# Performance work log

Hardware: AMD Instinct MI355X
Metric: run time of the kernel (lower is better)

## Reference

```python
import jax, jax.numpy as jnp
import numpy as np

N_NODES = 100000
N_EDGES = 1600000
IN_FEATS = 128
H_FEATS = 64
NUM_CLASSES = 16


def setup_inputs() -> dict:
    key = jax.random.key(0)
    ks = jax.random.split(key, 6)
    X = jax.random.normal(ks[0], (N_NODES, IN_FEATS), dtype=jnp.float32)
    edge_weight = jax.random.uniform(ks[1], (N_EDGES,), dtype=jnp.float32)
    W1 = jax.random.normal(ks[2], (IN_FEATS, H_FEATS), dtype=jnp.float32) * (1.0 / np.sqrt(IN_FEATS))
    b1 = jnp.zeros((H_FEATS,), dtype=jnp.float32)
    W2 = jax.random.normal(ks[3], (H_FEATS, NUM_CLASSES), dtype=jnp.float32) * (1.0 / np.sqrt(H_FEATS))
    b2 = jnp.zeros((NUM_CLASSES,), dtype=jnp.float32)
    edge_src = jax.random.randint(ks[4], (N_EDGES,), 0, N_NODES, dtype=jnp.int32)
    edge_dst = jax.random.randint(ks[5], (N_EDGES,), 0, N_NODES, dtype=jnp.int32)
    return {"X": X, "edge_weight": edge_weight, "W1": W1, "b1": b1,
            "W2": W2, "b2": b2, "edge_src": edge_src, "edge_dst": edge_dst}


def _gcn_conv(H, W, b, edge_src, edge_dst, edge_weight, num_nodes):
    # transform-then-aggregate: out = A @ (H @ W) + b, A given as weighted edge list
    H = H @ W                                  # [N, d_out]
    msgs = H[edge_src] * edge_weight[:, None]  # [E, d_out] gather + scale
    agg = jax.ops.segment_sum(msgs, edge_dst, num_segments=num_nodes)  # scatter-add
    return agg + b


def reference(X, edge_weight, W1, b1, W2, b2, edge_src, edge_dst):
    n = X.shape[0]
    h = jax.nn.relu(_gcn_conv(X, W1, b1, edge_src, edge_dst, edge_weight, n))
    return _gcn_conv(h, W2, b2, edge_src, edge_dst, edge_weight, n)
```

## Files before the change

kernel.cpp:

```cpp
#include <hip/hip_runtime.h>

#define N_NODES 100000
#define N_EDGES 1600000
#define IN_F 128
#define H_F 64
#define C_F 16

#define BIN_SH 7
#define BIN_NODES 128
#define NBINS 782
#define BCAP 2816
#define PART_BLOCKS 391
#define GEMM1_BLOCKS 1563
#define RMAX 6

typedef __attribute__((ext_vector_type(8))) short bf16x8;
typedef __attribute__((ext_vector_type(4))) float f32x4;

__device__ inline unsigned short f2bf(float f) {
  unsigned u = __float_as_uint(f);
  unsigned r = (u + 0x7fff + ((u >> 16) & 1)) >> 16;
  return (unsigned short)r;
}

__global__ __launch_bounds__(256) void part_gemm1_kernel(
    const int* __restrict__ src, const int* __restrict__ dst,
    const float* __restrict__ ew, int* __restrict__ binCnt,
    int2* __restrict__ ebin, const float* __restrict__ X,
    const float* __restrict__ W1, unsigned short* __restrict__ H1b) {
  __shared__ char ldsraw[16 * 1024];
  int tid = threadIdx.x;
  if (blockIdx.x < PART_BLOCKS) {
    int* hist = (int*)ldsraw;
    int* base = hist + NBINS;
    for (int i = tid; i < NBINS; i += 256) hist[i] = 0;
    __syncthreads();
    int i0 = blockIdx.x * 1024;
    int iHi = i0 + 1024;
    if (iHi > N_EDGES / 4) iHi = N_EDGES / 4;
    const int4* d4p = (const int4*)dst;
    const int4* s4p = (const int4*)src;
    const float4* w4p = (const float4*)ew;
    unsigned key[16];
    unsigned aux[16];
#pragma unroll
    for (int it = 0; it < 4; ++it) {
      int i = i0 + it * 256 + tid;
      if (i < iHi) {
        int4 d = d4p[i];
        int4 s = s4p[i];
        float4 w = w4p[i];
#pragma unroll
        for (int j = 0; j < 4; ++j) {
          int dd = (&d.x)[j];
          int ss = (&s.x)[j];
          float ww = (&w.x)[j];
          int bb = dd >> BIN_SH;
          unsigned wf = (unsigned)(ww * 32767.0f + 0.5f);
          key[it * 4 + j] =
              (unsigned)ss | ((unsigned)(dd & (BIN_NODES - 1)) << 17);
          aux[it * 4 + j] = wf | ((unsigned)bb << 15);
          atomicAdd(&hist[bb], 1);
        }
      }
    }
    __syncthreads();
    for (int i = tid; i < NBINS; i += 256)
      base[i] = hist[i] ? atomicAdd(&binCnt[i], hist[i]) : 0;
    __syncthreads();
#pragma unroll
    for (int it = 0; it < 4; ++it) {
      int i = i0 + it * 256 + tid;
      if (i < iHi) {
#pragma unroll
        for (int j = 0; j < 4; ++j) {
          unsigned a = aux[it * 4 + j];
          int bb = (int)(a >> 15);
          int pos = atomicAdd(&base[bb], 1);
          ebin[(size_t)bb * BCAP + pos] =
              make_int2((int)key[it * 4 + j], (int)(a & 0x7FFF));
        }
      }
    }
  } else {
    short* ldsB = (short*)ldsraw;
    for (int idx = tid; idx < 16 * 512; idx += 256) {
      int frag = idx >> 9;
      int entry = idx & 511;
      int lane = entry >> 3, j = entry & 7;
      int c = frag >> 2, s = frag & 3;
      int k = s * 32 + (lane >> 4) * 8 + j;
      int n = c * 16 + (lane & 15);
      ldsB[idx] = (short)f2bf(W1[k * H_F + n]);
    }
    __syncthreads();
    int wave = tid >> 6;
    int lane = tid & 63;
    int rt = (blockIdx.x - PART_BLOCKS) * 4 + wave;
    if (rt >= N_NODES / 16) return;
    int node0 = rt * 16;
    int l = lane & 15, q = lane >> 4;
    const float* xp = X + (size_t)(node0 + l) * IN_F + q * 8;
    f32x4 acc[4] = {f32x4{0.f, 0.f, 0.f, 0.f}, f32x4{0.f, 0.f, 0.f, 0.f},
                    f32x4{0.f, 0.f, 0.f, 0.f}, f32x4{0.f, 0.f, 0.f, 0.f}};
#pragma unroll
    for (int s = 0; s < 4; ++s) {
      float4 x0 = *(const float4*)(xp + s * 32);
      float4 x1 = *(const float4*)(xp + s * 32 + 4);
      bf16x8 a;
      a[0] = f2bf(x0.x); a[1] = f2bf(x0.y); a[2] = f2bf(x0.z); a[3] = f2bf(x0.w);
      a[4] = f2bf(x1.x); a[5] = f2bf(x1.y); a[6] = f2bf(x1.z); a[7] = f2bf(x1.w);
#pragma unroll
      for (int c = 0; c < 4; ++c) {
        bf16x8 b = *(const bf16x8*)&ldsB[(c * 4 + s) * 512 + lane * 8];
        acc[c] = __builtin_amdgcn_mfma_f32_16x16x32_bf16(a, b, acc[c], 0, 0, 0);
      }
    }
#pragma unroll
    for (int c = 0; c < 4; ++c)
#pragma unroll
      for (int r = 0; r < 4; ++r)
        H1b[(size_t)(node0 + q * 4 + r) * H_F + c * 16 + l] = f2bf(acc[c][r]);
  }
}

__global__ __launch_bounds__(512) void gather1s_kernel(
    const uint2* __restrict__ H1q, const int* __restrict__ binCnt,
    const int2* __restrict__ ebin, const float* __restrict__ b1,
    float* __restrict__ agg) {
  __shared__ int h[BIN_NODES], sc[BIN_NODES], cur[BIN_NODES];
  __shared__ unsigned srt[BCAP];
  int b = blockIdx.x, tid = threadIdx.x;
  int lo = b * BCAP;
  int cnt = binCnt[b];
  if (tid < BIN_NODES) h[tid] = 0;
  __syncthreads();
  unsigned rk[RMAX];
  int rd[RMAX];
  int rn = 0;
#pragma unroll
  for (int j = 0; j < RMAX; ++j) {
    int e = j * 512 + tid;
    if (e < cnt) {
      int2 r = ebin[lo + e];
      int dl = (((unsigned)r.x) >> 17) & (BIN_NODES - 1);
      rk[j] = ((unsigned)r.x & 0x1FFFF) | ((unsigned)r.y << 17);
      rd[j] = dl;
      atomicAdd(&h[dl], 1);
      rn = j + 1;
    }
  }
  __syncthreads();
  if (tid < BIN_NODES) sc[tid] = h[tid];
  __syncthreads();
#pragma unroll
  for (int d = 1; d < BIN_NODES; d <<= 1) {
    int t = 0;
    if (tid < BIN_NODES && tid >= d) t = sc[tid - d];
    __syncthreads();
    if (tid < BIN_NODES) sc[tid] += t;
    __syncthreads();
  }
  if (tid < BIN_NODES) cur[tid] = sc[tid] - h[tid];
  __syncthreads();
#pragma unroll
  for (int j = 0; j < RMAX; ++j)
    if (j < rn) {
      int pos = atomicAdd(&cur[rd[j]], 1);
      srt[pos] = rk[j];
    }
  __syncthreads();
  int wv = tid >> 6, lane = tid & 63, g = lane >> 4, li = lane & 15;
  const float wsc = 1.0f / 32767.0f;
  float bb0 = b1[li * 4], bb1 = b1[li * 4 + 1];
  float bb2 = b1[li * 4 + 2], bb3 = b1[li * 4 + 3];
  for (int k = 0; k < 16; ++k) {
    int nl = wv * 16 + k;
    int n = (b << BIN_SH) + nl;
    if (n >= N_NODES) break;
    int e1 = sc[nl], e0 = e1 - h[nl];
    f32x4 a0 = {0.f, 0.f, 0.f, 0.f}, a1 = {0.f, 0.f, 0.f, 0.f};
    f32x4 a2 = {0.f, 0.f, 0.f, 0.f}, a3 = {0.f, 0.f, 0.f, 0.f};
    int i = e0;
    for (; i + 15 < e1; i += 16) {
      unsigned r0 = srt[i + g];
      unsigned r1 = srt[i + 4 + g];
      unsigned r2 = srt[i + 8 + g];
      unsigned r3 = srt[i + 12 + g];
      uint2 v0 = H1q[(r0 & 0x1FFFF) * (H_F / 4) + li];
      uint2 v1 = H1q[(r1 & 0x1FFFF) * (H_F / 4) + li];
      uint2 v2 = H1q[(r2 & 0x1FFFF) * (H_F / 4) + li];
      uint2 v3 = H1q[(r3 & 0x1FFFF) * (H_F / 4) + li];
      float w0 = (float)(r0 >> 17) * wsc, w1 = (float)(r1 >> 17) * wsc;
      float w2 = (float)(r2 >> 17) * wsc, w3 = (float)(r3 >> 17) * wsc;
      a0[0] += __uint_as_float(v0.x << 16) * w0;
      a0[1] += __uint_as_float(v0.x & 0xFFFF0000u) * w0;
      a0[2] += __uint_as_float(v0.y << 16) * w0;
      a0[3] += __uint_as_float(v0.y & 0xFFFF0000u) * w0;
      a1[0] += __uint_as_float(v1.x << 16) * w1;
      a1[1] += __uint_as_float(v1.x & 0xFFFF0000u) * w1;
      a1[2] += __uint_as_float(v1.y << 16) * w1;
      a1[3] += __uint_as_float(v1.y & 0xFFFF0000u) * w1;
      a2[0] += __uint_as_float(v2.x << 16) * w2;
      a2[1] += __uint_as_float(v2.x & 0xFFFF0000u) * w2;
      a2[2] += __uint_as_float(v2.y << 16) * w2;
      a2[3] += __uint_as_float(v2.y & 0xFFFF0000u) * w2;
      a3[0] += __uint_as_float(v3.x << 16) * w3;
      a3[1] += __uint_as_float(v3.x & 0xFFFF0000u) * w3;
      a3[2] += __uint_as_float(v3.y << 16) * w3;
      a3[3] += __uint_as_float(v3.y & 0xFFFF0000u) * w3;
    }
    for (; i + 3 < e1; i += 4) {
      unsigned r0 = srt[i + g];
      uint2 v0 = H1q[(r0 & 0x1FFFF) * (H_F / 4) + li];
      float w0 = (float)(r0 >> 17) * wsc;
      a0[0] += __uint_as_float(v0.x << 16) * w0;
      a0[1] += __uint_as_float(v0.x & 0xFFFF0000u) * w0;
      a0[2] += __uint_as_float(v0.y << 16) * w0;
      a0[3] += __uint_as_float(v0.y & 0xFFFF0000u) * w0;
    }
    if (i + g < e1) {
      unsigned r0 = srt[i + g];
      uint2 v0 = H1q[(r0 & 0x1FFFF) * (H_F / 4) + li];
      float w0 = (float)(r0 >> 17) * wsc;
      a1[0] += __uint_as_float(v0.x << 16) * w0;
      a1[1] += __uint_as_float(v0.x & 0xFFFF0000u) * w0;
      a1[2] += __uint_as_float(v0.y << 16) * w0;
      a1[3] += __uint_as_float(v0.y & 0xFFFF0000u) * w0;
    }
    f32x4 a = (a0 + a1) + (a2 + a3);
#pragma unroll
    for (int c = 0; c < 4; ++c) {
      a[c] += __shfl_xor(a[c], 16, 64);
      a[c] += __shfl_xor(a[c], 32, 64);
    }
    if (g == 0) {
      float4 o;
      o.x = a[0] + bb0;
      o.y = a[1] + bb1;
      o.z = a[2] + bb2;
      o.w = a[3] + bb3;
      *(float4*)&agg[(size_t)n * H_F + li * 4] = o;
    }
  }
}

__global__ __launch_bounds__(256) void gemm2_mfma_kernel(
    const float* __restrict__ agg, const float* __restrict__ W2,
    unsigned short* __restrict__ H2b) {
  __shared__ short ldsB[2 * 512];
  for (int idx = threadIdx.x; idx < 1024; idx += 256) {
    int sfrag = idx >> 9;
    int entry = idx & 511;
    int lane = entry >> 3, j = entry & 7;
    int k = sfrag * 32 + (lane >> 4) * 8 + j;
    int c = lane & 15;
    ldsB[idx] = (short)f2bf(W2[k * C_F + c]);
  }
  __syncthreads();
  int wave = threadIdx.x >> 6;
  int lane = threadIdx.x & 63;
  int rt = blockIdx.x * 4 + wave;
  if (rt >= N_NODES / 16) return;
  int node0 = rt * 16;
  int l = lane & 15, q = lane >> 4;
  const float* ap = agg + (size_t)(node0 + l) * H_F + q * 8;
  f32x4 acc = {0.f, 0.f, 0.f, 0.f};
#pragma unroll
  for (int s = 0; s < 2; ++s) {
    float4 x0 = *(const float4*)(ap + s * 32);
    float4 x1 = *(const float4*)(ap + s * 32 + 4);
    bf16x8 a;
    a[0] = f2bf(fmaxf(x0.x, 0.f)); a[1] = f2bf(fmaxf(x0.y, 0.f));
    a[2] = f2bf(fmaxf(x0.z, 0.f)); a[3] = f2bf(fmaxf(x0.w, 0.f));
    a[4] = f2bf(fmaxf(x1.x, 0.f)); a[5] = f2bf(fmaxf(x1.y, 0.f));
    a[6] = f2bf(fmaxf(x1.z, 0.f)); a[7] = f2bf(fmaxf(x1.w, 0.f));
    bf16x8 bfr = *(const bf16x8*)&ldsB[s * 512 + lane * 8];
    acc = __builtin_amdgcn_mfma_f32_16x16x32_bf16(a, bfr, acc, 0, 0, 0);
  }
#pragma unroll
  for (int r = 0; r < 4; ++r)
    H2b[(size_t)(node0 + q * 4 + r) * C_F + l] = f2bf(acc[r]);
}

__global__ __launch_bounds__(512) void gather2s_kernel(
    const uint2* __restrict__ H2q, const int* __restrict__ binCnt,
    const int2* __restrict__ ebin, const float* __restrict__ b2,
    float* __restrict__ out) {
  __shared__ int h[BIN_NODES], sc[BIN_NODES], cur[BIN_NODES];
  __shared__ unsigned srt[BCAP];
  int b = blockIdx.x, tid = threadIdx.x;
  int lo = b * BCAP;
  int cnt = binCnt[b];
  if (tid < BIN_NODES) h[tid] = 0;
  __syncthreads();
  unsigned rk[RMAX];
  int rd[RMAX];
  int rn = 0;
#pragma unroll
  for (int j = 0; j < RMAX; ++j) {
    int e = j * 512 + tid;
    if (e < cnt) {
      int2 r = ebin[lo + e];
      int dl = (((unsigned)r.x) >> 17) & (BIN_NODES - 1);
      rk[j] = ((unsigned)r.x & 0x1FFFF) | ((unsigned)r.y << 17);
      rd[j] = dl;
      atomicAdd(&h[dl], 1);
      rn = j + 1;
    }
  }
  __syncthreads();
  if (tid < BIN_NODES) sc[tid] = h[tid];
  __syncthreads();
#pragma unroll
  for (int d = 1; d < BIN_NODES; d <<= 1) {
    int t = 0;
    if (tid < BIN_NODES && tid >= d) t = sc[tid - d];
    __syncthreads();
    if (tid < BIN_NODES) sc[tid] += t;
    __syncthreads();
  }
  if (tid < BIN_NODES) cur[tid] = sc[tid] - h[tid];
  __syncthreads();
#pragma unroll
  for (int j = 0; j < RMAX; ++j)
    if (j < rn) {
      int pos = atomicAdd(&cur[rd[j]], 1);
      srt[pos] = rk[j];
    }
  __syncthreads();
  int wv = tid >> 6, lane = tid & 63, g = lane >> 2, li = lane & 3;
  const float wsc = 1.0f / 32767.0f;
  float bb0 = b2[li * 4], bb1 = b2[li * 4 + 1];
  float bb2 = b2[li * 4 + 2], bb3 = b2[li * 4 + 3];
  for (int k = 0; k < 16; ++k) {
    int nl = wv * 16 + k;
    int n = (b << BIN_SH) + nl;
    if (n >= N_NODES) break;
    int e1 = sc[nl], e0 = e1 - h[nl];
    f32x4 a0 = {0.f, 0.f, 0.f, 0.f};
    int i = e0;
    for (; i + 15 < e1; i += 16) {
      unsigned r0 = srt[i + g];
      uint2 v0 = H2q[(r0 & 0x1FFFF) * (C_F / 4) + li];
      float w0 = (float)(r0 >> 17) * wsc;
      a0[0] += __uint_as_float(v0.x << 16) * w0;
      a0[1] += __uint_as_float(v0.x & 0xFFFF0000u) * w0;
      a0[2] += __uint_as_float(v0.y << 16) * w0;
      a0[3] += __uint_as_float(v0.y & 0xFFFF0000u) * w0;
    }
    if (i + g < e1) {
      unsigned r0 = srt[i + g];
      uint2 v0 = H2q[(r0 & 0x1FFFF) * (C_F / 4) + li];
      float w0 = (float)(r0 >> 17) * wsc;
      a0[0] += __uint_as_float(v0.x << 16) * w0;
      a0[1] += __uint_as_float(v0.x & 0xFFFF0000u) * w0;
      a0[2] += __uint_as_float(v0.y << 16) * w0;
      a0[3] += __uint_as_float(v0.y & 0xFFFF0000u) * w0;
    }
#pragma unroll
    for (int c = 0; c < 4; ++c) {
      a0[c] += __shfl_xor(a0[c], 4, 64);
      a0[c] += __shfl_xor(a0[c], 8, 64);
      a0[c] += __shfl_xor(a0[c], 16, 64);
      a0[c] += __shfl_xor(a0[c], 32, 64);
    }
    if (g == 0) {
      float4 o;
      o.x = a0[0] + bb0;
      o.y = a0[1] + bb1;
      o.z = a0[2] + bb2;
      o.w = a0[3] + bb3;
      *(float4*)&out[(size_t)n * C_F + li * 4] = o;
    }
  }
}

extern "C" void kernel_launch(void* const* d_in, const int* in_sizes, int n_in,
                              void* d_out, int out_size, void* d_ws,
                              size_t ws_size, hipStream_t stream) {
  const float* X  = (const float*)d_in[0];
  const float* ew = (const float*)d_in[1];
  const float* W1 = (const float*)d_in[2];
  const float* b1 = (const float*)d_in[3];
  const float* W2 = (const float*)d_in[4];
  const float* b2 = (const float*)d_in[5];
  const int* src  = (const int*)d_in[6];
  const int* dst  = (const int*)d_in[7];
  float* out = (float*)d_out;

  unsigned short* H1b = (unsigned short*)d_ws;
  float* agg  = (float*)((char*)d_ws + (size_t)N_NODES * H_F * 2);
  int2* ebin  = (int2*)((char*)agg + (size_t)N_NODES * H_F * 4);
  int* binCnt = (int*)(ebin + (size_t)NBINS * BCAP);
  unsigned short* H2b = H1b;

  hipMemsetAsync(binCnt, 0, NBINS * sizeof(int), stream);
  part_gemm1_kernel<<<PART_BLOCKS + GEMM1_BLOCKS, 256, 0, stream>>>(
      src, dst, ew, binCnt, ebin, X, W1, H1b);
  gather1s_kernel<<<NBINS, 512, 0, stream>>>((const uint2*)H1b, binCnt, ebin,
                                             b1, agg);
  gemm2_mfma_kernel<<<(N_NODES / 16 + 3) / 4, 256, 0, stream>>>(agg, W2, H2b);
  gather2s_kernel<<<NBINS, 512, 0, stream>>>((const uint2*)H2b, binCnt, ebin,
                                             b2, out);
}
```

Measured before the change: 218.4 us.

## Fuse layer-2 GEMM into layer-1 gather kernel via LDS staging

The layer-1 aggregation kernel now keeps each bin's 128 aggregated node rows in LDS as bias-added, ReLU'd bf16 values. It then runs the 64x16 W2 MFMA directly on them and writes H2 in bf16. This drops the separate gemm2 kernel launch and the round trip of the fp32 agg buffer through global memory (about 25.6 MB written and read). In exchange it adds LDS use (about 18 KB extra per block), which may lower occupancy of the gather kernel, and moves H2b to its own workspace region.

Result: faster. 213.6 us (-2.2%).

```diff
diff --git a/kernel.cpp b/kernel.cpp
--- a/kernel.cpp
+++ b/kernel.cpp
@@ -13,6 +13,7 @@
 #define PART_BLOCKS 391
 #define GEMM1_BLOCKS 1563
 #define RMAX 6
+#define AGG_STRIDE 36
 
 typedef __attribute__((ext_vector_type(8))) short bf16x8;
 typedef __attribute__((ext_vector_type(4))) float f32x4;
@@ -124,13 +125,23 @@
   }
 }
 
-__global__ __launch_bounds__(512) void gather1s_kernel(
+__global__ __launch_bounds__(512) void gather1f_kernel(
     const uint2* __restrict__ H1q, const int* __restrict__ binCnt,
     const int2* __restrict__ ebin, const float* __restrict__ b1,
-    float* __restrict__ agg) {
+    const float* __restrict__ W2, unsigned short* __restrict__ H2b) {
   __shared__ int h[BIN_NODES], sc[BIN_NODES], cur[BIN_NODES];
   __shared__ unsigned srt[BCAP];
+  __shared__ unsigned aggU[BIN_NODES * AGG_STRIDE];
+  __shared__ short ldsW2[2 * 512];
   int b = blockIdx.x, tid = threadIdx.x;
+  for (int idx = tid; idx < 1024; idx += 512) {
+    int sfrag = idx >> 9;
+    int entry = idx & 511;
+    int lane = entry >> 3, j = entry & 7;
+    int k = sfrag * 32 + (lane >> 4) * 8 + j;
+    int c = lane & 15;
+    ldsW2[idx] = (short)f2bf(W2[k * C_F + c]);
+  }
   int lo = b * BCAP;
   int cnt = binCnt[b];
   if (tid < BIN_NODES) h[tid] = 0;
@@ -235,52 +246,31 @@
       a[c] += __shfl_xor(a[c], 32, 64);
     }
     if (g == 0) {
-      float4 o;
-      o.x = a[0] + bb0;
-      o.y = a[1] + bb1;
-      o.z = a[2] + bb2;
-      o.w = a[3] + bb3;
-      *(float4*)&agg[(size_t)n * H_F + li * 4] = o;
-    }
-  }
-}
-
-__global__ __launch_bounds__(256) void gemm2_mfma_kernel(
-    const float* __restrict__ agg, const float* __restrict__ W2,
-    unsigned short* __restrict__ H2b) {
-  __shared__ short ldsB[2 * 512];
-  for (int idx = threadIdx.x; idx < 1024; idx += 256) {
-    int sfrag = idx >> 9;
-    int entry = idx & 511;
-    int lane = entry >> 3, j = entry & 7;
-    int k = sfrag * 32 + (lane >> 4) * 8 + j;
-    int c = lane & 15;
-    ldsB[idx] = (short)f2bf(W2[k * C_F + c]);
-  }
-  __syncthreads();
-  int wave = threadIdx.x >> 6;
-  int lane = threadIdx.x & 63;
-  int rt = blockIdx.x * 4 + wave;
-  if (rt >= N_NODES / 16) return;
-  int node0 = rt * 16;
+      float r0 = fmaxf(a[0] + bb0, 0.f);
+      float r1 = fmaxf(a[1] + bb1, 0.f);
+      float r2 = fmaxf(a[2] + bb2, 0.f);
+      float r3 = fmaxf(a[3] + bb3, 0.f);
+      unsigned p0 = (unsigned)f2bf(r0) | ((unsigned)f2bf(r1) << 16);
+      unsigned p1 = (unsigned)f2bf(r2) | ((unsigned)f2bf(r3) << 16);
+      *(uint2*)&aggU[nl * AGG_STRIDE + li * 2] = make_uint2(p0, p1);
+    }
+  }
+  __syncthreads();
   int l = lane & 15, q = lane >> 4;
-  const float* ap = agg + (size_t)(node0 + l) * H_F + q * 8;
+  int nl0 = wv * 16;
   f32x4 acc = {0.f, 0.f, 0.f, 0.f};
 #pragma unroll
   for (int s = 0; s < 2; ++s) {
-    float4 x0 = *(const float4*)(ap + s * 32);
-    float4 x1 = *(const float4*)(ap + s * 32 + 4);
-    bf16x8 a;
-    a[0] = f2bf(fmaxf(x0.x, 0.f)); a[1] = f2bf(fmaxf(x0.y, 0.f));
-    a[2] = f2bf(fmaxf(x0.z, 0.f)); a[3] = f2bf(fmaxf(x0.w, 0.f));
-    a[4] = f2bf(fmaxf(x1.x, 0.f)); a[5] = f2bf(fmaxf(x1.y, 0.f));
-    a[6] = f2bf(fmaxf(x1.z, 0.f)); a[7] = f2bf(fmaxf(x1.w, 0.f));
-    bf16x8 bfr = *(const bf16x8*)&ldsB[s * 512 + lane * 8];
-    acc = __builtin_amdgcn_mfma_f32_16x16x32_bf16(a, bfr, acc, 0, 0, 0);
-  }
-#pragma unroll
-  for (int r = 0; r < 4; ++r)
-    H2b[(size_t)(node0 + q * 4 + r) * C_F + l] = f2bf(acc[r]);
+    bf16x8 afr = *(const bf16x8*)&aggU[(nl0 + l) * AGG_STRIDE + s * 16 + q * 4];
+    bf16x8 bfr = *(const bf16x8*)&ldsW2[s * 512 + lane * 8];
+    acc = __builtin_amdgcn_mfma_f32_16x16x32_bf16(afr, bfr, acc, 0, 0, 0);
+  }
+  int node0 = (b << BIN_SH) + nl0;
+#pragma unroll
+  for (int r = 0; r < 4; ++r) {
+    int n = node0 + q * 4 + r;
+    if (n < N_NODES) H2b[(size_t)n * C_F + l] = f2bf(acc[r]);
+  }
 }
 
 __global__ __launch_bounds__(512) void gather2s_kernel(
@@ -390,17 +380,15 @@
   float* out = (float*)d_out;
 
   unsigned short* H1b = (unsigned short*)d_ws;
-  float* agg  = (float*)((char*)d_ws + (size_t)N_NODES * H_F * 2);
-  int2* ebin  = (int2*)((char*)agg + (size_t)N_NODES * H_F * 4);
+  unsigned short* H2b = H1b + (size_t)N_NODES * H_F;
+  int2* ebin  = (int2*)(H2b + (size_t)N_NODES * C_F);
   int* binCnt = (int*)(ebin + (size_t)NBINS * BCAP);
-  unsigned short* H2b = H1b;
 
   hipMemsetAsync(binCnt, 0, NBINS * sizeof(int), stream);
   part_gemm1_kernel<<<PART_BLOCKS + GEMM1_BLOCKS, 256, 0, stream>>>(
       src, dst, ew, binCnt, ebin, X, W1, H1b);
-  gather1s_kernel<<<NBINS, 512, 0, stream>>>((const uint2*)H1b, binCnt, ebin,
-                                             b1, agg);
-  gemm2_mfma_kernel<<<(N_NODES / 16 + 3) / 4, 256, 0, stream>>>(agg, W2, H2b);
+  gather1f_kernel<<<NBINS, 512, 0, stream>>>((const uint2*)H1b, binCnt, ebin,
+                                             b1, W2, H2b);
   gather2s_kernel<<<NBINS, 512, 0, stream>>>((const uint2*)H2b, binCnt, ebin,
                                              b2, out);
 }
```
